# Kernel tuning notes

Hardware: AMD Instinct MI355X
Metric: run time of the kernel (lower is better)

## Reference

```python
import jax, jax.numpy as jnp
import numpy as np
from jax.scipy.special import logsumexp

TEMPERATURE = 0.1
BETA = 0.999
EPS = 1e-8
HARD_K = 10  # min(num_classes // 4, 10) with num_classes = 1000


def _l2norm(x, axis=-1):
    return x * jax.lax.rsqrt(jnp.sum(x * x, axis=axis, keepdims=True) + 1e-24)


def setup_inputs() -> dict:
    key = jax.random.key(0)
    k1, k2, k3, k4, k5 = jax.random.split(key, 5)
    B, D, C, M = 4096, 1024, 1000, 32768
    return {
        "image_features": jax.random.normal(k1, (B, D), dtype=jnp.float32),
        "prompts": jax.random.normal(k2, (C, D), dtype=jnp.float32),
        "labels": jax.random.randint(k3, (B, C), 0, 2, dtype=jnp.int32),
        "memory_features": jax.random.normal(k4, (M, D), dtype=jnp.float32),
        "memory_labels": jax.random.randint(k5, (M, C), 0, 2, dtype=jnp.int32),
        "mem_ptr": 16384,
    }


def reference(image_features, prompts, labels, memory_features, memory_labels, mem_ptr):
    B, D = image_features.shape
    C = prompts.shape[0]
    labels_f = labels.astype(jnp.float32)

    # z_img = F.normalize(image_features)
    z_img = _l2norm(image_features, axis=1)

    # class weights (effective-number reweighting), computed from this batch's labels
    counts = labels_f.sum(axis=0)                              # [C]
    effective_num = 1.0 - jnp.power(jnp.float32(BETA), counts)
    weights = (1.0 - BETA) / (effective_num + EPS)
    weights = weights / jnp.sum(weights) * C                   # [C]

    # memory bank update (detached write of current batch at ptr), then use [:ptr+B]
    mem_f = memory_features.at[mem_ptr:mem_ptr + B].set(jax.lax.stop_gradient(z_img))
    mem_l = memory_labels.at[mem_ptr:mem_ptr + B].set(labels)
    used = mem_ptr + B  # static

    enhanced_features = jnp.concatenate([z_img, mem_f[:used]], axis=0)     # [N, D]
    enhanced_labels = jnp.concatenate([labels_f, mem_l[:used].astype(jnp.float32)], axis=0)  # [N, C]

    z_prompts = _l2norm(prompts, axis=1)                       # [C, D]
    sim = (enhanced_features @ z_prompts.T) / TEMPERATURE      # [N, C]

    pos_mask = enhanced_labels > 0                             # [N, C]

    # hard negatives: top-K similarities among negatives define the keep threshold
    sim_for_neg = jnp.where(pos_mask, -jnp.inf, sim)
    hard_neg_vals, _ = jax.lax.top_k(sim_for_neg, HARD_K)      # [N, K]
    min_hard_neg = hard_neg_vals[:, -1:]                       # [N, 1]
    neg_mask = (~pos_mask) & (sim >= min_hard_neg)
    full_mask = pos_mask | neg_mask

    lse = logsumexp(jnp.where(full_mask, sim, -jnp.inf), axis=1)  # [N]
    log_prob = sim - lse[:, None]                              # [N, C]

    posf = pos_mask.astype(sim.dtype)
    pos_w = posf * weights[None, :]                            # [N, C]
    weight_sums = pos_w.sum(axis=1)                            # [N]
    loss_num = (pos_w * (-log_prob)).sum(axis=1)               # [N]

    valid = weight_sums > 0
    loss_per_sample = jnp.where(valid, loss_num / (weight_sums + EPS), 0.0)
    n_valid = jnp.maximum(valid.sum(), 1)
    attr_loss = loss_per_sample.sum() / n_valid.astype(sim.dtype)
    # single attribute -> total_loss / num_valid_attrs == attr_loss
    return attr_loss
```

## Files before the change

### kernel.cpp

```cpp
#include <hip/hip_runtime.h>
#include <math.h>

#define BN    4096
#define DD    1024
#define CC    1000
#define MM    32768
#define ROWS_CAP 32768
#define SIMLD 1024

typedef __attribute__((ext_vector_type(8))) short short8;
typedef __attribute__((ext_vector_type(4))) short short4v;
typedef __attribute__((ext_vector_type(4))) float f32x4;

__device__ __forceinline__ float wave_max_f(float v) {
#pragma unroll
  for (int off = 32; off >= 1; off >>= 1) v = fmaxf(v, __shfl_xor(v, off, 64));
  return v;
}
__device__ __forceinline__ float wave_sum_f(float v) {
#pragma unroll
  for (int off = 32; off >= 1; off >>= 1) v += __shfl_xor(v, off, 64);
  return v;
}

__device__ __forceinline__ short f2bf(float f) {
  union { float f; unsigned u; } v; v.f = f;
  unsigned r = v.u + 0x7FFF + ((v.u >> 16) & 1);
  return (short)(r >> 16);
}
__device__ __forceinline__ float bf2f(unsigned short u) {
  union { unsigned u; float f; } v; v.u = ((unsigned)u) << 16;
  return v.f;
}

__device__ __forceinline__ void gload16(const short* g, short* l) {
  __builtin_amdgcn_global_load_lds(
      (const __attribute__((address_space(1))) unsigned int*)g,
      (__attribute__((address_space(3))) unsigned int*)l, 16, 0, 0);
}

__global__ __launch_bounds__(256) void count_kernel(const int* __restrict__ labels,
                                                    int* __restrict__ counts) {
  const int c = blockIdx.x * 256 + threadIdx.x;
  if (c >= CC) return;
  const int b0 = blockIdx.y * 64;
  int s = 0;
  for (int b = b0; b < b0 + 64; ++b) s += labels[(size_t)b * CC + c];
  atomicAdd(&counts[c], s);
}

__global__ __launch_bounds__(1024) void weights_kernel(const int* __restrict__ counts,
                                                       float* __restrict__ weights) {
  const int t = threadIdx.x;
  float w = 0.f;
  if (t < CC) {
    float cnt = (float)counts[t];
    float en = 1.0f - expf(cnt * logf(0.999f));
    w = (1.0f - 0.999f) / (en + 1e-8f);
  }
  float s = wave_sum_f(w);
  __shared__ float part[16];
  if ((t & 63) == 0) part[t >> 6] = s;
  __syncthreads();
  float tot = 0.f;
#pragma unroll
  for (int i = 0; i < 16; ++i) tot += part[i];
  if (t < CC) weights[t] = w * ((float)CC / tot);
}

__global__ __launch_bounds__(256) void conv_kernel(const float* __restrict__ img,
                                                   const float* __restrict__ prompts,
                                                   const float* __restrict__ mem,
                                                   const int* __restrict__ memptr,
                                                   short* __restrict__ A,
                                                   short* __restrict__ B) {
  __shared__ float part[4];
  const int t = threadIdx.x;
  const int blk = blockIdx.x;
  if (blk >= ROWS_CAP) {
    const int row = blk - ROWS_CAP;
    short4v o = {0, 0, 0, 0};
    if (row < CC) {
      float4 v = ((const float4*)(prompts + (size_t)row * DD))[t];
      float s = v.x * v.x + v.y * v.y + v.z * v.z + v.w * v.w;
      s = wave_sum_f(s);
      if ((t & 63) == 0) part[t >> 6] = s;
      __syncthreads();
      float sc = 10.0f * rsqrtf(part[0] + part[1] + part[2] + part[3] + 1e-24f);
      o[0] = f2bf(v.x * sc); o[1] = f2bf(v.y * sc);
      o[2] = f2bf(v.z * sc); o[3] = f2bf(v.w * sc);
    }
    ((short4v*)(B + (size_t)row * DD))[t] = o;
    return;
  }
  const int nrows = BN + memptr[0];
  const int padded = (nrows + 127) & ~127;
  const int row = blk;
  if (row >= padded) return;
  short4v o = {0, 0, 0, 0};
  if (row < nrows) {
    const float* src = (row < BN) ? img + (size_t)row * DD
                                  : mem + (size_t)(row - BN) * DD;
    float4 v = ((const float4*)src)[t];
    float sc = 1.0f;
    if (row < BN) {
      float s = v.x * v.x + v.y * v.y + v.z * v.z + v.w * v.w;
      s = wave_sum_f(s);
      if ((t & 63) == 0) part[t >> 6] = s;
      __syncthreads();
      sc = rsqrtf(part[0] + part[1] + part[2] + part[3] + 1e-24f);
    }
    o[0] = f2bf(v.x * sc); o[1] = f2bf(v.y * sc);
    o[2] = f2bf(v.z * sc); o[3] = f2bf(v.w * sc);
  }
  ((short4v*)(A + (size_t)row * DD))[t] = o;
}

__global__ __launch_bounds__(256) void gemm_mfma(const short* __restrict__ A,
                                                 const short* __restrict__ Bm,
                                                 const int* __restrict__ memptr,
                                                 short* __restrict__ simbf, int lo) {
  const int f = blockIdx.x;
  const int x = f & 7;
  const int s = f >> 3;
  const int c = s & 7;
  const int rt = (s >> 3) * 8 + x;

  const int nrows = BN + memptr[0];
  const int row0 = rt * 128;
  if (lo + row0 >= nrows) return;
  const int c0 = c * 128;

  __shared__ short As[128 * 64];
  __shared__ short Bs[128 * 64];

  const int t = threadIdx.x;
  const int lane = t & 63;
  const int wid = t >> 6;
  const int wm = (wid >> 1) * 64;
  const int wn = (wid & 1) * 64;

  const int srow = t >> 3;
  const int gchunk = (t & 7) ^ (srow & 7);
  const short* ga = A + (size_t)(lo + row0 + srow) * DD + gchunk * 8;
  const short* gb = Bm + (size_t)(c0 + srow) * DD + gchunk * 8;
  short* lA = As + t * 8;
  short* lB = Bs + t * 8;

  f32x4 acc[4][4] = {};
  const int lm = lane & 15;
  const int q0 = lane >> 4;

  for (int k0 = 0; k0 < DD; k0 += 64) {
#pragma unroll
    for (int p = 0; p < 4; ++p) gload16(ga + (size_t)(p * 32) * DD + k0, lA + p * 2048);
#pragma unroll
    for (int p = 0; p < 4; ++p) gload16(gb + (size_t)(p * 32) * DD + k0, lB + p * 2048);
    __syncthreads();
#pragma unroll
    for (int kk = 0; kk < 2; ++kk) {
      short8 af[4], bfr[4];
      const int qc = q0 + kk * 4;
#pragma unroll
      for (int i = 0; i < 4; ++i) {
        int m = wm + i * 16 + lm;
        af[i] = *(const short8*)(As + m * 64 + ((qc ^ (m & 7)) * 8));
      }
#pragma unroll
      for (int i = 0; i < 4; ++i) {
        int n = wn + i * 16 + lm;
        bfr[i] = *(const short8*)(Bs + n * 64 + ((qc ^ (n & 7)) * 8));
      }
#pragma unroll
      for (int mi = 0; mi < 4; ++mi)
#pragma unroll
        for (int ni = 0; ni < 4; ++ni)
          acc[mi][ni] = __builtin_amdgcn_mfma_f32_16x16x32_bf16(af[mi], bfr[ni], acc[mi][ni], 0, 0, 0);
    }
    __syncthreads();
  }

  const int rbase = row0 + wm + (lane >> 4) * 4;
#pragma unroll
  for (int ni = 0; ni < 4; ++ni) {
    const int col = c0 + wn + ni * 16 + lm;
#pragma unroll
    for (int mi = 0; mi < 4; ++mi) {
      f32x4 v = acc[mi][ni];
      const int rl = rbase + mi * 16;
#pragma unroll
      for (int r = 0; r < 4; ++r)
        simbf[(size_t)(rl + r) * SIMLD + col] = f2bf(v[r]);
    }
  }
}

__global__ __launch_bounds__(256) void rowpost_kernel(
    const short* __restrict__ simbf, const int* __restrict__ labels,
    const int* __restrict__ mlabels, const float* __restrict__ weights,
    const int* __restrict__ memptr, float* __restrict__ lps_arr,
    float* __restrict__ valid_arr, int chunk_lo) {
  __shared__ float wlds[1024];
  {
    const int t = threadIdx.x;
#pragma unroll
    for (int i = 0; i < 4; ++i) {
      int c = t + i * 256;
      wlds[c] = (c < CC) ? weights[c] : 0.f;
    }
  }
  __syncthreads();

  const int nrows = BN + memptr[0];
  const int wid = threadIdx.x >> 6;
  const int lane = threadIdx.x & 63;
  const int row = chunk_lo + blockIdx.x * 4 + wid;
  if (row >= ROWS_CAP) return;
  if (row >= nrows) {
    if (lane == 0) { lps_arr[row] = 0.f; valid_arr[row] = 0.f; }
    return;
  }

  const unsigned short* srow = (const unsigned short*)simbf + (size_t)(row - chunk_lo) * SIMLD;
  const int* lrow = (row < BN) ? labels + (size_t)row * CC
                               : mlabels + (size_t)(row - BN) * CC;
  float sv[16];
  bool pv[16];
  float vneg[16];
#pragma unroll
  for (int j = 0; j < 16; ++j) {
    int c = lane + 64 * j;
    bool ok = (c < CC);
    float s = ok ? bf2f(srow[c]) : -INFINITY;
    bool p = ok && (lrow[c] > 0);
    sv[j] = ok ? s : -INFINITY;
    pv[j] = p;
    vneg[j] = (ok && !p) ? s : -INFINITY;
  }

  float v10 = -INFINITY;
  for (int r = 0; r < 10; ++r) {
    float lmx = -INFINITY;
#pragma unroll
    for (int j = 0; j < 16; ++j) lmx = fmaxf(lmx, vneg[j]);
    lmx = wave_max_f(lmx);
#pragma unroll
    for (int j = 0; j < 16; ++j) if (vneg[j] == lmx) vneg[j] = -INFINITY;
    v10 = lmx;
  }

  float mmax = -INFINITY;
#pragma unroll
  for (int j = 0; j < 16; ++j) {
    if (pv[j] || sv[j] >= v10) mmax = fmaxf(mmax, sv[j]);
  }
  mmax = wave_max_f(mmax);

  float esum = 0.f, wsum = 0.f, wsim = 0.f;
#pragma unroll
  for (int j = 0; j < 16; ++j) {
    int c = lane + 64 * j;
    if (c < CC) {
      if (pv[j] || sv[j] >= v10) esum += expf(sv[j] - mmax);
      if (pv[j]) { float w = wlds[c]; wsum += w; wsim += w * sv[j]; }
    }
  }
  esum = wave_sum_f(esum);
  wsum = wave_sum_f(wsum);
  wsim = wave_sum_f(wsim);

  if (lane == 0) {
    float lse = mmax + logf(esum);
    bool valid = (wsum > 0.f);
    float lps = valid ? (wsum * lse - wsim) / (wsum + 1e-8f) : 0.f;
    float mult = (row < BN) ? 2.f : 1.f;
    lps_arr[row] = mult * lps;
    valid_arr[row] = valid ? mult : 0.f;
  }
}

__global__ __launch_bounds__(1024) void reduce_kernel(const float* __restrict__ lps_arr,
                                                      const float* __restrict__ valid_arr,
                                                      float* __restrict__ out) {
  const int t = threadIdx.x;
  const float4* l4 = (const float4*)lps_arr;
  const float4* v4 = (const float4*)valid_arr;
  float s1 = 0.f, s2 = 0.f;
#pragma unroll
  for (int i = 0; i < 8; ++i) {
    float4 a = l4[t + i * 1024];
    float4 b = v4[t + i * 1024];
    s1 += a.x + a.y + a.z + a.w;
    s2 += b.x + b.y + b.z + b.w;
  }
  s1 = wave_sum_f(s1);
  s2 = wave_sum_f(s2);
  __shared__ float p1[16], p2[16];
  if ((t & 63) == 0) { p1[t >> 6] = s1; p2[t >> 6] = s2; }
  __syncthreads();
  if (t == 0) {
    float a = 0.f, b = 0.f;
#pragma unroll
    for (int i = 0; i < 16; ++i) { a += p1[i]; b += p2[i]; }
    out[0] = a / fmaxf(b, 1.0f);
  }
}

extern "C" void kernel_launch(void* const* d_in, const int* in_sizes, int n_in,
                              void* d_out, int out_size, void* d_ws, size_t ws_size,
                              hipStream_t stream) {
  const float* img     = (const float*)d_in[0];
  const float* prompts = (const float*)d_in[1];
  const int*   labels  = (const int*)d_in[2];
  const float* mem     = (const float*)d_in[3];
  const int*   mlabels = (const int*)d_in[4];
  const int*   memptr  = (const int*)d_in[5];
  float* out = (float*)d_out;
  char* ws = (char*)d_ws;

  int*   counts  = (int*)(ws + 0);
  float* weights = (float*)(ws + 4096);
  float* lps_arr = (float*)(ws + 8192);
  float* val_arr = (float*)(ws + 139264);
  short* Bbf     = (short*)(ws + 270336);
  short* Abf     = (short*)(ws + 2367488);
  const size_t fixed = 2367488 + (size_t)ROWS_CAP * DD * 2;
  short* simbf   = (short*)(ws + fixed);

  long long avail = (long long)ws_size - (long long)fixed;
  int chunk = (int)(avail / (SIMLD * 2));
  chunk &= ~1023;
  if (chunk < 1024) chunk = 1024;
  if (chunk > ROWS_CAP) chunk = ROWS_CAP;

  hipMemsetAsync(ws, 0, 4096, stream);

  conv_kernel<<<ROWS_CAP + 1024, 256, 0, stream>>>(img, prompts, mem, memptr, Abf, Bbf);
  count_kernel<<<dim3((CC + 255) / 256, BN / 64), 256, 0, stream>>>(labels, counts);
  weights_kernel<<<1, 1024, 0, stream>>>(counts, weights);

  for (int lo = 0; lo < ROWS_CAP; lo += chunk) {
    int rows = (ROWS_CAP - lo < chunk) ? (ROWS_CAP - lo) : chunk;
    int rowTiles = rows / 128;
    gemm_mfma<<<8 * rowTiles, 256, 0, stream>>>(Abf, Bbf, memptr, simbf, lo);
    rowpost_kernel<<<rows / 4, 256, 0, stream>>>(simbf, labels, mlabels, weights, memptr,
                                                 lps_arr, val_arr, lo);
  }
  reduce_kernel<<<1, 1024, 0, stream>>>(lps_arr, val_arr, out);
}
```

Before: 355.5 us.

## Switch similarity GEMM to FP8 scaled MFMA and vectorize rowpost loads

Converts normalized features and prompts to packed FP8 instead of bf16 and computes the similarity GEMM with the 32x32x64 f8f6f4 scaled MFMA, using a new LDS layout with K-chunk-major staging. This halves operand bytes for conversion writes and GEMM loads and doubles MFMA throughput, at the risk of lower precision in the similarities, which feed the top-k threshold and the loss. The row post-processing also switches to contiguous per-lane column ownership, so the sim and label reads become vector loads instead of strided scalar loads.

```diff
diff --git a/kernel.cpp b/kernel.cpp
--- a/kernel.cpp
+++ b/kernel.cpp
@@ -8,9 +8,8 @@
 #define ROWS_CAP 32768
 #define SIMLD 1024
 
-typedef __attribute__((ext_vector_type(8))) short short8;
-typedef __attribute__((ext_vector_type(4))) short short4v;
-typedef __attribute__((ext_vector_type(4))) float f32x4;
+typedef __attribute__((ext_vector_type(8))) int   int8v;
+typedef __attribute__((ext_vector_type(16))) float f32x16;
 
 __device__ __forceinline__ float wave_max_f(float v) {
 #pragma unroll
@@ -33,7 +32,7 @@
   return v.f;
 }
 
-__device__ __forceinline__ void gload16(const short* g, short* l) {
+__device__ __forceinline__ void gload16(const unsigned char* g, unsigned char* l) {
   __builtin_amdgcn_global_load_lds(
       (const __attribute__((address_space(1))) unsigned int*)g,
       (__attribute__((address_space(3))) unsigned int*)l, 16, 0, 0);
@@ -72,14 +71,14 @@
                                                    const float* __restrict__ prompts,
                                                    const float* __restrict__ mem,
                                                    const int* __restrict__ memptr,
-                                                   short* __restrict__ A,
-                                                   short* __restrict__ B) {
+                                                   unsigned char* __restrict__ A,
+                                                   unsigned char* __restrict__ B) {
   __shared__ float part[4];
   const int t = threadIdx.x;
   const int blk = blockIdx.x;
   if (blk >= ROWS_CAP) {
     const int row = blk - ROWS_CAP;
-    short4v o = {0, 0, 0, 0};
+    int packed = 0;
     if (row < CC) {
       float4 v = ((const float4*)(prompts + (size_t)row * DD))[t];
       float s = v.x * v.x + v.y * v.y + v.z * v.z + v.w * v.w;
@@ -87,17 +86,17 @@
       if ((t & 63) == 0) part[t >> 6] = s;
       __syncthreads();
       float sc = 10.0f * rsqrtf(part[0] + part[1] + part[2] + part[3] + 1e-24f);
-      o[0] = f2bf(v.x * sc); o[1] = f2bf(v.y * sc);
-      o[2] = f2bf(v.z * sc); o[3] = f2bf(v.w * sc);
-    }
-    ((short4v*)(B + (size_t)row * DD))[t] = o;
+      packed = __builtin_amdgcn_cvt_pk_fp8_f32(v.x * sc, v.y * sc, 0, false);
+      packed = __builtin_amdgcn_cvt_pk_fp8_f32(v.z * sc, v.w * sc, packed, true);
+    }
+    ((int*)(B + (size_t)row * DD))[t] = packed;
     return;
   }
   const int nrows = BN + memptr[0];
   const int padded = (nrows + 127) & ~127;
   const int row = blk;
   if (row >= padded) return;
-  short4v o = {0, 0, 0, 0};
+  int packed = 0;
   if (row < nrows) {
     const float* src = (row < BN) ? img + (size_t)row * DD
                                   : mem + (size_t)(row - BN) * DD;
@@ -110,16 +109,16 @@
       __syncthreads();
       sc = rsqrtf(part[0] + part[1] + part[2] + part[3] + 1e-24f);
     }
-    o[0] = f2bf(v.x * sc); o[1] = f2bf(v.y * sc);
-    o[2] = f2bf(v.z * sc); o[3] = f2bf(v.w * sc);
-  }
-  ((short4v*)(A + (size_t)row * DD))[t] = o;
-}
-
-__global__ __launch_bounds__(256) void gemm_mfma(const short* __restrict__ A,
-                                                 const short* __restrict__ Bm,
-                                                 const int* __restrict__ memptr,
-                                                 short* __restrict__ simbf, int lo) {
+    packed = __builtin_amdgcn_cvt_pk_fp8_f32(v.x * sc, v.y * sc, 0, false);
+    packed = __builtin_amdgcn_cvt_pk_fp8_f32(v.z * sc, v.w * sc, packed, true);
+  }
+  ((int*)(A + (size_t)row * DD))[t] = packed;
+}
+
+__global__ __launch_bounds__(256) void gemm_mx(const unsigned char* __restrict__ A,
+                                               const unsigned char* __restrict__ Bm,
+                                               const int* __restrict__ memptr,
+                                               short* __restrict__ simbf, int lo) {
   const int f = blockIdx.x;
   const int x = f & 7;
   const int s = f >> 3;
@@ -131,8 +130,8 @@
   if (lo + row0 >= nrows) return;
   const int c0 = c * 128;
 
-  __shared__ short As[128 * 64];
-  __shared__ short Bs[128 * 64];
+  __shared__ unsigned char As[16384];
+  __shared__ unsigned char Bs[16384];
 
   const int t = threadIdx.x;
   const int lane = t & 63;
@@ -140,59 +139,70 @@
   const int wm = (wid >> 1) * 64;
   const int wn = (wid & 1) * 64;
 
-  const int srow = t >> 3;
-  const int gchunk = (t & 7) ^ (srow & 7);
-  const short* ga = A + (size_t)(lo + row0 + srow) * DD + gchunk * 8;
-  const short* gb = Bm + (size_t)(c0 + srow) * DD + gchunk * 8;
-  short* lA = As + t * 8;
-  short* lB = Bs + t * 8;
-
-  f32x4 acc[4][4] = {};
-  const int lm = lane & 15;
-  const int q0 = lane >> 4;
-
-  for (int k0 = 0; k0 < DD; k0 += 64) {
-#pragma unroll
-    for (int p = 0; p < 4; ++p) gload16(ga + (size_t)(p * 32) * DD + k0, lA + p * 2048);
-#pragma unroll
-    for (int p = 0; p < 4; ++p) gload16(gb + (size_t)(p * 32) * DD + k0, lB + p * 2048);
+  const int r_st = t & 127;
+  const int kc_hi = t >> 7;
+  const unsigned char* gaB = A + (size_t)(lo + row0 + r_st) * DD;
+  const unsigned char* gbB = Bm + (size_t)(c0 + r_st) * DD;
+  unsigned char* lA = As + t * 16;
+  unsigned char* lB = Bs + t * 16;
+
+  f32x16 acc[2][2] = {};
+  const int q = lane >> 5;
+  const int rr = lane & 31;
+
+  for (int k0 = 0; k0 < DD; k0 += 128) {
+#pragma unroll
+    for (int p = 0; p < 4; ++p)
+      gload16(gaB + k0 + (p * 2 + kc_hi) * 16, lA + p * 4096);
+#pragma unroll
+    for (int p = 0; p < 4; ++p)
+      gload16(gbB + k0 + (p * 2 + kc_hi) * 16, lB + p * 4096);
     __syncthreads();
 #pragma unroll
-    for (int kk = 0; kk < 2; ++kk) {
-      short8 af[4], bfr[4];
-      const int qc = q0 + kk * 4;
-#pragma unroll
-      for (int i = 0; i < 4; ++i) {
-        int m = wm + i * 16 + lm;
-        af[i] = *(const short8*)(As + m * 64 + ((qc ^ (m & 7)) * 8));
+    for (int h = 0; h < 2; ++h) {
+      int8v af[2], bfv[2];
+      const int kc = h * 4 + q * 2;
+#pragma unroll
+      for (int mi = 0; mi < 2; ++mi) {
+        const unsigned char* pa = As + kc * 2048 + (wm + mi * 32 + rr) * 16;
+        int4 lo4 = *(const int4*)pa;
+        int4 hi4 = *(const int4*)(pa + 2048);
+        af[mi][0] = lo4.x; af[mi][1] = lo4.y; af[mi][2] = lo4.z; af[mi][3] = lo4.w;
+        af[mi][4] = hi4.x; af[mi][5] = hi4.y; af[mi][6] = hi4.z; af[mi][7] = hi4.w;
       }
 #pragma unroll
-      for (int i = 0; i < 4; ++i) {
-        int n = wn + i * 16 + lm;
-        bfr[i] = *(const short8*)(Bs + n * 64 + ((qc ^ (n & 7)) * 8));
+      for (int ni = 0; ni < 2; ++ni) {
+        const unsigned char* pb = Bs + kc * 2048 + (wn + ni * 32 + rr) * 16;
+        int4 lo4 = *(const int4*)pb;
+        int4 hi4 = *(const int4*)(pb + 2048);
+        bfv[ni][0] = lo4.x; bfv[ni][1] = lo4.y; bfv[ni][2] = lo4.z; bfv[ni][3] = lo4.w;
+        bfv[ni][4] = hi4.x; bfv[ni][5] = hi4.y; bfv[ni][6] = hi4.z; bfv[ni][7] = hi4.w;
       }
 #pragma unroll
-      for (int mi = 0; mi < 4; ++mi)
-#pragma unroll
-        for (int ni = 0; ni < 4; ++ni)
-          acc[mi][ni] = __builtin_amdgcn_mfma_f32_16x16x32_bf16(af[mi], bfr[ni], acc[mi][ni], 0, 0, 0);
+      for (int mi = 0; mi < 2; ++mi)
+#pragma unroll
+        for (int ni = 0; ni < 2; ++ni)
+          acc[mi][ni] = __builtin_amdgcn_mfma_scale_f32_32x32x64_f8f6f4(
+              af[mi], bfv[ni], acc[mi][ni], 0, 0, 0, 127, 0, 127);
     }
     __syncthreads();
   }
 
-  const int rbase = row0 + wm + (lane >> 4) * 4;
-#pragma unroll
-  for (int ni = 0; ni < 4; ++ni) {
-    const int col = c0 + wn + ni * 16 + lm;
-#pragma unroll
-    for (int mi = 0; mi < 4; ++mi) {
-      f32x4 v = acc[mi][ni];
-      const int rl = rbase + mi * 16;
-#pragma unroll
-      for (int r = 0; r < 4; ++r)
-        simbf[(size_t)(rl + r) * SIMLD + col] = f2bf(v[r]);
-    }
-  }
+  const int cl = lane & 31;
+  const int r4 = 4 * (lane >> 5);
+#pragma unroll
+  for (int mi = 0; mi < 2; ++mi)
+#pragma unroll
+    for (int ni = 0; ni < 2; ++ni) {
+      f32x16 v = acc[mi][ni];
+      const int colg = c0 + wn + ni * 32 + cl;
+      const int rbase = row0 + wm + mi * 32 + r4;
+#pragma unroll
+      for (int reg = 0; reg < 16; ++reg) {
+        const int rowl = rbase + (reg & 3) + 8 * (reg >> 2);
+        simbf[(size_t)rowl * SIMLD + colg] = f2bf(v[reg]);
+      }
+    }
 }
 
 __global__ __launch_bounds__(256) void rowpost_kernel(
@@ -224,18 +234,35 @@
   const unsigned short* srow = (const unsigned short*)simbf + (size_t)(row - chunk_lo) * SIMLD;
   const int* lrow = (row < BN) ? labels + (size_t)row * CC
                                : mlabels + (size_t)(row - BN) * CC;
+  const int cbase = lane * 16;
+
+  unsigned short sraw[16];
+  *(ulonglong2*)&sraw[0] = *(const ulonglong2*)(srow + cbase);
+  *(ulonglong2*)&sraw[8] = *(const ulonglong2*)(srow + cbase + 8);
+  int lab[16];
+#pragma unroll
+  for (int g = 0; g < 4; ++g) {
+    int c = cbase + g * 4;
+    if (c + 3 < CC) {
+      *(int4*)&lab[g * 4] = *(const int4*)(lrow + c);
+    } else {
+#pragma unroll
+      for (int u = 0; u < 4; ++u) lab[g * 4 + u] = (c + u < CC) ? lrow[c + u] : 0;
+    }
+  }
+
   float sv[16];
   bool pv[16];
   float vneg[16];
 #pragma unroll
   for (int j = 0; j < 16; ++j) {
-    int c = lane + 64 * j;
+    int c = cbase + j;
     bool ok = (c < CC);
-    float s = ok ? bf2f(srow[c]) : -INFINITY;
-    bool p = ok && (lrow[c] > 0);
-    sv[j] = ok ? s : -INFINITY;
+    float sf = bf2f(sraw[j]);
+    bool p = ok && (lab[j] > 0);
+    sv[j] = ok ? sf : -INFINITY;
     pv[j] = p;
-    vneg[j] = (ok && !p) ? s : -INFINITY;
+    vneg[j] = (ok && !p) ? sf : -INFINITY;
   }
 
   float v10 = -INFINITY;
@@ -259,7 +286,7 @@
   float esum = 0.f, wsum = 0.f, wsim = 0.f;
 #pragma unroll
   for (int j = 0; j < 16; ++j) {
-    int c = lane + 64 * j;
+    int c = cbase + j;
     if (c < CC) {
       if (pv[j] || sv[j] >= v10) esum += expf(sv[j] - mmax);
       if (pv[j]) { float w = wlds[c]; wsum += w; wsim += w * sv[j]; }
@@ -322,10 +349,10 @@
   float* weights = (float*)(ws + 4096);
   float* lps_arr = (float*)(ws + 8192);
   float* val_arr = (float*)(ws + 139264);
-  short* Bbf     = (short*)(ws + 270336);
-  short* Abf     = (short*)(ws + 2367488);
-  const size_t fixed = 2367488 + (size_t)ROWS_CAP * DD * 2;
-  short* simbf   = (short*)(ws + fixed);
+  unsigned char* Bf8 = (unsigned char*)(ws + 270336);
+  unsigned char* Af8 = (unsigned char*)(ws + 1318912);
+  const size_t fixed = 1318912 + (size_t)ROWS_CAP * DD;
+  short* simbf = (short*)(ws + fixed);
 
   long long avail = (long long)ws_size - (long long)fixed;
   int chunk = (int)(avail / (SIMLD * 2));
@@ -335,14 +362,14 @@
 
   hipMemsetAsync(ws, 0, 4096, stream);
 
-  conv_kernel<<<ROWS_CAP + 1024, 256, 0, stream>>>(img, prompts, mem, memptr, Abf, Bbf);
+  conv_kernel<<<ROWS_CAP + 1024, 256, 0, stream>>>(img, prompts, mem, memptr, Af8, Bf8);
   count_kernel<<<dim3((CC + 255) / 256, BN / 64), 256, 0, stream>>>(labels, counts);
   weights_kernel<<<1, 1024, 0, stream>>>(counts, weights);
 
   for (int lo = 0; lo < ROWS_CAP; lo += chunk) {
     int rows = (ROWS_CAP - lo < chunk) ? (ROWS_CAP - lo) : chunk;
     int rowTiles = rows / 128;
-    gemm_mfma<<<8 * rowTiles, 256, 0, stream>>>(Abf, Bbf, memptr, simbf, lo);
+    gemm_mx<<<8 * rowTiles, 256, 0, stream>>>(Af8, Bf8, memptr, simbf, lo);
     rowpost_kernel<<<rows / 4, 256, 0, stream>>>(simbf, labels, mlabels, weights, memptr,
                                                  lps_arr, val_arr, lo);
   }
```

New measurement: 351.7 us. Within noise of the previous version (-1.1%).
